# Performance work log

Measured on AMD Instinct MI355X. Metric: run time of the kernel, lower is better.

Reference implementation:

```python
import jax, jax.numpy as jnp
import numpy as np

B, S, D, H, E, K = 2, 2048, 1024, 4096, 8, 2


def setup_inputs() -> dict:
    key = jax.random.key(0)
    ks = jax.random.split(key, 5)
    x = jax.random.normal(ks[0], (B, S, D), dtype=jnp.float32)
    W = 0.02 * jax.random.normal(ks[1], (H, D), dtype=jnp.float32)
    bias = 0.02 * jax.random.normal(ks[2], (H,), dtype=jnp.float32)
    # alpha initialized near 1 (nn.Parameter(torch.ones(...)) + learned perturbation)
    alpha = 1.0 + 0.02 * jax.random.normal(ks[3], (E, D), dtype=jnp.float32)
    beta = 0.02 * jax.random.normal(ks[4], (E, D), dtype=jnp.float32)
    return {"x": x, "W": W, "bias": bias, "alpha": alpha, "beta": beta}


def reference(x, W, bias, alpha, beta):
    """MoEXLayer eval-mode forward (sparsity-aware routing + expert combine).

    x: [B,S,D], W: [H,D], bias: [H], alpha/beta: [E,D]. Returns [B,S,H].
    """
    E = alpha.shape[0]
    # --- Router: per-virtual-expert Gaussian pre-activation statistics ---
    # reconstructed_weight(alpha, beta) = W * alpha + beta  (column-wise affine)
    W_rec = W[None, :, :] * alpha[:, None, :] + beta[:, None, :]      # [E,H,D]
    mu_w = W_rec.mean(axis=1)                                          # [E,D]
    var_w = W_rec.var(axis=1)                                          # [E,D] (unbiased=False)
    mu_h = jnp.einsum('bsd,ed->bse', x, mu_w) + bias.mean()            # [B,S,E]
    sigma_h = jnp.sqrt(jnp.einsum('bsd,ed->bse', x * x, var_w) + 1e-8) # [B,S,E]
    router_logits = jax.lax.erf(mu_h / (jnp.sqrt(2.0) * sigma_h))      # [B,S,E]

    # --- Top-k routing: softmax over top-k logits, zeros elsewhere ---
    topk_vals, topk_idx = jax.lax.top_k(router_logits, K)              # [B,S,K]
    topk_w = jax.nn.softmax(topk_vals, axis=-1)                        # [B,S,K]
    router_weights = (jax.nn.one_hot(topk_idx, E, dtype=x.dtype)
                      * topk_w[..., None]).sum(axis=-2)                # [B,S,E]

    # --- Expert compute + combine (dispatch passes alpha only => beta=0) ---
    W_disp = W[None, :, :] * alpha[:, None, :]                         # [E,H,D]
    pre = jnp.einsum('bsd,ehd->bseh', x, W_disp) + bias                # [B,S,E,H]
    expert_out = jax.nn.relu(pre)
    out = jnp.einsum('bseh,bse->bsh', expert_out, router_weights)      # [B,S,H]
    return out
```

## Files before the change

kernel.cpp:

```cpp
#include <hip/hip_runtime.h>
#include <hip/hip_bf16.h>
#include <math.h>

#define DD 1024
#define HH 4096
#define EE 8
#define MTOK 4096
#define MROWS 8192

typedef __attribute__((ext_vector_type(8))) short bf16x8;
typedef __attribute__((ext_vector_type(4))) float f32x4;

__device__ __forceinline__ unsigned short f2bf(float x){
  __hip_bfloat16 h = __float2bfloat16(x);
  return *reinterpret_cast<unsigned short*>(&h);
}

__device__ __forceinline__ void gload16(const void* g, void* l){
  __builtin_amdgcn_global_load_lds((__attribute__((address_space(1))) void*)g,
                                   (__attribute__((address_space(3))) void*)l,
                                   16, 0, 0);
}

__global__ void cvtstats_kernel(const float4* __restrict__ W4, ushort4* __restrict__ Wb4,
                                float* __restrict__ pmean, float* __restrict__ pm2){
  int rc = blockIdx.x;
  int tid = threadIdx.x;
  double s0=0,s1=0,s2_=0,s3=0, q0=0,q1=0,q2=0,q3=0;
  for (int h = rc * 16; h < rc * 16 + 16; ++h){
    float4 w = W4[(size_t)h * 256 + tid];
    Wb4[(size_t)h * 256 + tid] = make_ushort4(f2bf(w.x), f2bf(w.y), f2bf(w.z), f2bf(w.w));
    s0 += w.x; q0 += (double)w.x * w.x;
    s1 += w.y; q1 += (double)w.y * w.y;
    s2_ += w.z; q2 += (double)w.z * w.z;
    s3 += w.w; q3 += (double)w.w * w.w;
  }
  int d0 = rc * DD + tid * 4;
  pmean[d0]   = (float)s0;  pm2[d0]   = (float)q0;
  pmean[d0+1] = (float)s1;  pm2[d0+1] = (float)q1;
  pmean[d0+2] = (float)s2_; pm2[d0+2] = (float)q2;
  pmean[d0+3] = (float)s3;  pm2[d0+3] = (float)q3;
}

__global__ void finalize_kernel(const float* __restrict__ pmean, const float* __restrict__ pm2,
                                const float* __restrict__ bias,
                                const float* __restrict__ alpha, const float* __restrict__ beta,
                                double* __restrict__ bmean,
                                float* __restrict__ muw, float* __restrict__ vw){
  __shared__ double redS[4][64], redQ[4][64], redB[256];
  int tid = threadIdx.x;
  int dlane = tid & 63, cq = tid >> 6;
  int d = blockIdx.x * 64 + dlane;
  double s = 0.0, s2 = 0.0;
  for (int c = cq * 64; c < cq * 64 + 64; ++c){
    s  += (double)pmean[c * DD + d];
    s2 += (double)pm2[c * DD + d];
  }
  redS[cq][dlane] = s; redQ[cq][dlane] = s2;
  __syncthreads();
  if (cq == 0){
    double S  = redS[0][dlane] + redS[1][dlane] + redS[2][dlane] + redS[3][dlane];
    double Q  = redQ[0][dlane] + redQ[1][dlane] + redQ[2][dlane] + redQ[3][dlane];
    double m = S / (double)HH;
    double v = Q / (double)HH - m * m;
    #pragma unroll
    for (int e = 0; e < EE; ++e){
      double a = (double)alpha[e * DD + d];
      muw[e * DD + d] = (float)(a * m + (double)beta[e * DD + d]);
      vw[e * DD + d]  = (float)(a * a * v);
    }
  }
  if (blockIdx.x == 0){
    double bs = 0.0;
    for (int h = tid; h < HH; h += 256) bs += (double)bias[h];
    redB[tid] = bs;
    __syncthreads();
    for (int k = 128; k > 0; k >>= 1){
      if (tid < k) redB[tid] += redB[tid + k];
      __syncthreads();
    }
    if (tid == 0) *bmean = redB[0] / (double)HH;
  }
}

__global__ __launch_bounds__(256) void router_kernel(const float4* __restrict__ x4,
                                                     const float4* __restrict__ alpha4,
                                                     const float4* __restrict__ muw4,
                                                     const float4* __restrict__ vw4,
                                                     const double* __restrict__ bmeanp,
                                                     unsigned short* __restrict__ Xs,
                                                     float2* __restrict__ wpair){
  int wv = threadIdx.x >> 6, lane = threadIdx.x & 63;
  int t = blockIdx.x * 4 + wv;
  const float4* xt = x4 + (size_t)t * 256;

  float4 xv[4];
  double mu[EE], s2[EE];
  #pragma unroll
  for (int e = 0; e < EE; ++e){ mu[e] = 0.0; s2[e] = 0.0; }

  #pragma unroll
  for (int r = 0; r < 4; ++r){
    int c = lane + 64 * r;
    float4 xf = xt[c];
    xv[r] = xf;
    float x2x = xf.x * xf.x, x2y = xf.y * xf.y, x2z = xf.z * xf.z, x2w = xf.w * xf.w;
    #pragma unroll
    for (int e = 0; e < EE; ++e){
      float4 m4 = muw4[e * 256 + c];
      float4 v4 = vw4[e * 256 + c];
      mu[e] += (double)xf.x * m4.x + (double)xf.y * m4.y
             + (double)xf.z * m4.z + (double)xf.w * m4.w;
      s2[e] += (double)x2x * v4.x + (double)x2y * v4.y
             + (double)x2z * v4.z + (double)x2w * v4.w;
    }
  }

  #pragma unroll
  for (int off = 32; off > 0; off >>= 1){
    #pragma unroll
    for (int e = 0; e < EE; ++e){
      mu[e] += __shfl_xor(mu[e], off);
      s2[e] += __shfl_xor(s2[e], off);
    }
  }

  double bm = *bmeanp;
  double z[EE];
  #pragma unroll
  for (int e = 0; e < EE; ++e){
    double m = mu[e] + bm;
    double v = s2[e] + 1e-8;
    z[e] = m / sqrt(2.0 * v);
  }
  int e1 = 0;
  #pragma unroll
  for (int e = 1; e < EE; ++e) if (z[e] > z[e1]) e1 = e;
  int e2 = -1;
  #pragma unroll
  for (int e = 0; e < EE; ++e){
    if (e == e1) continue;
    if (e2 < 0 || z[e] > z[e2]) e2 = e;
  }
  double lg1 = erf(z[e1]), lg2 = erf(z[e2]);
  double ex = exp(lg2 - lg1);
  float w1 = (float)(1.0 / (1.0 + ex));
  float w2 = (float)(ex / (1.0 + ex));
  if (lane == 0) wpair[t] = make_float2(w1, w2);

  const float4* a1 = alpha4 + (size_t)e1 * 256;
  const float4* a2 = alpha4 + (size_t)e2 * 256;
  ushort4* X1 = (ushort4*)(Xs + (size_t)(2 * t) * DD);
  ushort4* X2 = (ushort4*)(Xs + (size_t)(2 * t + 1) * DD);
  #pragma unroll
  for (int r = 0; r < 4; ++r){
    int c = lane + 64 * r;
    float4 xf = xv[r];
    float4 av = a1[c];
    X1[c] = make_ushort4(f2bf(xf.x * av.x), f2bf(xf.y * av.y),
                         f2bf(xf.z * av.z), f2bf(xf.w * av.w));
    av = a2[c];
    X2[c] = make_ushort4(f2bf(xf.x * av.x), f2bf(xf.y * av.y),
                         f2bf(xf.z * av.z), f2bf(xf.w * av.w));
  }
}

#define BM 256
#define BN 256
#define BKT 64
#define NKT (DD / BKT)
#define ASZ (BM * BKT)

__global__ __launch_bounds__(512, 1) void gemm_kernel(const unsigned short* __restrict__ Xs,
                                                      const unsigned short* __restrict__ Wb,
                                                      const float* __restrict__ bias,
                                                      const float2* __restrict__ wpair,
                                                      float* __restrict__ out){
  __shared__ __align__(16) unsigned short As[2 * ASZ];
  __shared__ __align__(16) unsigned short Bs[2 * ASZ];

  int tid = threadIdx.x, lane = tid & 63, wv = tid >> 6;
  int wr = wv >> 2, wc = wv & 3;
  int l15 = lane & 15;

  int bid = blockIdx.x;
  int ch = bid & 7, local = bid >> 3;
  int mtile = ch * 4 + (local & 3);
  int ntile = local >> 2;
  int bm0 = mtile * BM, bn0 = ntile * BN;

  int sr = tid >> 3;
  int sc = tid & 7;
  int scg = sc ^ (sr & 7);
  const unsigned short* gA = Xs + (size_t)(bm0 + sr) * DD + scg * 8;
  const unsigned short* gB = Wb + (size_t)(bn0 + sr) * DD + scg * 8;
  unsigned short* lA = As + tid * 8;
  unsigned short* lB = Bs + tid * 8;

  auto stage = [&](int kt, int slot){
    int koff = kt * BKT;
    #pragma unroll
    for (int j = 0; j < 4; ++j)
      gload16(gA + (size_t)(64 * j) * DD + koff, lA + slot * ASZ + j * 4096);
    #pragma unroll
    for (int j = 0; j < 4; ++j)
      gload16(gB + (size_t)(64 * j) * DD + koff, lB + slot * ASZ + j * 4096);
  };

  int r7 = l15 & 7;
  int posr0 = (lane >> 4) ^ r7;
  int posr1 = (4 + (lane >> 4)) ^ r7;

  f32x4 acc[8][4] = {};

  stage(0, 0);
  #pragma unroll 1
  for (int t = 0; t < NKT; ++t){
    int slot = t & 1;
    if (t < NKT - 1){
      stage(t + 1, slot ^ 1);
      asm volatile("s_waitcnt vmcnt(8)" ::: "memory");
    } else {
      asm volatile("s_waitcnt vmcnt(0)" ::: "memory");
    }
    __builtin_amdgcn_s_barrier();

    const unsigned short* Ab = As + slot * ASZ;
    const unsigned short* Bb = Bs + slot * ASZ;

    #pragma unroll
    for (int ks = 0; ks < 2; ++ks){
      int pos = ks ? posr1 : posr0;
      bf16x8 af[8], bfr[4];
      #pragma unroll
      for (int mi = 0; mi < 8; ++mi)
        af[mi] = *(const bf16x8*)(Ab + (wr * 128 + mi * 16 + l15) * BKT + pos * 8);
      #pragma unroll
      for (int ni = 0; ni < 4; ++ni)
        bfr[ni] = *(const bf16x8*)(Bb + (wc * 64 + ni * 16 + l15) * BKT + pos * 8);

      __builtin_amdgcn_s_setprio(1);
      #pragma unroll
      for (int ni = 0; ni < 4; ++ni)
        #pragma unroll
        for (int mi = 0; mi < 8; ++mi)
          acc[mi][ni] = __builtin_amdgcn_mfma_f32_16x16x32_bf16(af[mi], bfr[ni],
                                                               acc[mi][ni], 0, 0, 0);
      __builtin_amdgcn_s_setprio(0);
    }

    asm volatile("s_waitcnt lgkmcnt(0)" ::: "memory");
    __builtin_amdgcn_s_barrier();
  }

  #pragma unroll
  for (int mi = 0; mi < 8; ++mi){
    int rbase = bm0 + wr * 128 + mi * 16 + ((lane >> 4) << 2);
    #pragma unroll
    for (int jp = 0; jp < 2; ++jp){
      int gm = rbase + jp * 2;
      int tt = gm >> 1;
      float2 w = wpair[tt];
      #pragma unroll
      for (int ni = 0; ni < 4; ++ni){
        int gh = bn0 + wc * 64 + ni * 16 + l15;
        float bz = bias[gh];
        float v0 = acc[mi][ni][jp * 2]     + bz;
        float v1 = acc[mi][ni][jp * 2 + 1] + bz;
        out[(size_t)tt * HH + gh] = w.x * fmaxf(v0, 0.f) + w.y * fmaxf(v1, 0.f);
      }
    }
  }
}

extern "C" void kernel_launch(void* const* d_in, const int* in_sizes, int n_in,
                              void* d_out, int out_size, void* d_ws, size_t ws_size,
                              hipStream_t stream) {
  const float* x     = (const float*)d_in[0];
  const float* W     = (const float*)d_in[1];
  const float* bias  = (const float*)d_in[2];
  const float* alpha = (const float*)d_in[3];
  const float* beta  = (const float*)d_in[4];
  float* out = (float*)d_out;

  char* ws = (char*)d_ws;
  unsigned short* Wb = (unsigned short*)ws;
  unsigned short* Xs = (unsigned short*)(ws + (8u << 20));
  float2* wpair      = (float2*)(ws + (24u << 20));
  double* bmean      = (double*)(ws + (24u << 20) + (64u << 10));
  float* muw         = (float*)(ws + (24u << 20) + (128u << 10));
  float* vw          = muw + EE * DD;
  float* pmean       = (float*)(ws + (25u << 20));
  float* pm2         = (float*)(ws + (26u << 20));

  cvtstats_kernel<<<256, 256, 0, stream>>>((const float4*)W, (ushort4*)Wb, pmean, pm2);
  finalize_kernel<<<16, 256, 0, stream>>>(pmean, pm2, bias, alpha, beta, bmean, muw, vw);
  router_kernel<<<MTOK / 4, 256, 0, stream>>>((const float4*)x, (const float4*)alpha,
                                              (const float4*)muw, (const float4*)vw,
                                              bmean, Xs, wpair);
  gemm_kernel<<<(MROWS / BM) * (HH / BN), 512, 0, stream>>>(Xs, Wb, bias, wpair, out);
}
```

Measured before the change: 126.8 us.

## Split K tiles into half-stages and issue next loads after fragment reads

Each 64-wide K tile now sits in LDS as two 32-wide halves, laid out as [row][32] with a 4-way XOR swizzle. The next tile's global-to-LDS loads for a half are issued right after this wave reads its fragments for that half. A vmcnt(4) wait plus one barrier guards each half, and the trailing lgkmcnt wait and barrier at the end of each iteration are gone. The goal is to overlap loads with MFMA at a finer grain and cut synchronisation per tile. The risks are more LDS bank conflicts from the narrower swizzle and the cost of two barriers per tile.

```diff
diff --git a/kernel.cpp b/kernel.cpp
--- a/kernel.cpp
+++ b/kernel.cpp
@@ -169,15 +169,16 @@
 #define BN 256
 #define BKT 64
 #define NKT (DD / BKT)
-#define ASZ (BM * BKT)
+#define SLOTE 16384
+#define HALFE 8192
 
 __global__ __launch_bounds__(512, 1) void gemm_kernel(const unsigned short* __restrict__ Xs,
                                                       const unsigned short* __restrict__ Wb,
                                                       const float* __restrict__ bias,
                                                       const float2* __restrict__ wpair,
                                                       float* __restrict__ out){
-  __shared__ __align__(16) unsigned short As[2 * ASZ];
-  __shared__ __align__(16) unsigned short Bs[2 * ASZ];
+  __shared__ __align__(16) unsigned short As[2 * SLOTE];
+  __shared__ __align__(16) unsigned short Bs[2 * SLOTE];
 
   int tid = threadIdx.x, lane = tid & 63, wv = tid >> 6;
   int wr = wv >> 2, wc = wv & 3;
@@ -189,55 +190,51 @@
   int ntile = local >> 2;
   int bm0 = mtile * BM, bn0 = ntile * BN;
 
-  int sr = tid >> 3;
-  int sc = tid & 7;
-  int scg = sc ^ (sr & 7);
+  int sr = tid >> 2;
+  int sc = tid & 3;
+  int scg = sc ^ (sr & 3);
   const unsigned short* gA = Xs + (size_t)(bm0 + sr) * DD + scg * 8;
   const unsigned short* gB = Wb + (size_t)(bn0 + sr) * DD + scg * 8;
   unsigned short* lA = As + tid * 8;
   unsigned short* lB = Bs + tid * 8;
 
-  auto stage = [&](int kt, int slot){
-    int koff = kt * BKT;
-    #pragma unroll
-    for (int j = 0; j < 4; ++j)
-      gload16(gA + (size_t)(64 * j) * DD + koff, lA + slot * ASZ + j * 4096);
-    #pragma unroll
-    for (int j = 0; j < 4; ++j)
-      gload16(gB + (size_t)(64 * j) * DD + koff, lB + slot * ASZ + j * 4096);
+  auto stage = [&](int kt, int slot, int h){
+    int koff = kt * BKT + h * 32;
+    #pragma unroll
+    for (int j = 0; j < 2; ++j){
+      gload16(gA + (size_t)(128 * j) * DD + koff, lA + slot * SLOTE + h * HALFE + j * 4096);
+      gload16(gB + (size_t)(128 * j) * DD + koff, lB + slot * SLOTE + h * HALFE + j * 4096);
+    }
   };
 
-  int r7 = l15 & 7;
-  int posr0 = (lane >> 4) ^ r7;
-  int posr1 = (4 + (lane >> 4)) ^ r7;
+  int cc = ((lane >> 4) ^ (l15 & 3)) * 8;
 
   f32x4 acc[8][4] = {};
 
-  stage(0, 0);
+  stage(0, 0, 0);
+  stage(0, 0, 1);
+
   #pragma unroll 1
   for (int t = 0; t < NKT; ++t){
     int slot = t & 1;
-    if (t < NKT - 1){
-      stage(t + 1, slot ^ 1);
-      asm volatile("s_waitcnt vmcnt(8)" ::: "memory");
-    } else {
-      asm volatile("s_waitcnt vmcnt(0)" ::: "memory");
-    }
-    __builtin_amdgcn_s_barrier();
-
-    const unsigned short* Ab = As + slot * ASZ;
-    const unsigned short* Bb = Bs + slot * ASZ;
-
-    #pragma unroll
-    for (int ks = 0; ks < 2; ++ks){
-      int pos = ks ? posr1 : posr0;
+    const unsigned short* Ab = As + slot * SLOTE;
+    const unsigned short* Bb = Bs + slot * SLOTE;
+
+    #pragma unroll
+    for (int h = 0; h < 2; ++h){
+      if (t == NKT - 1 && h == 1) asm volatile("s_waitcnt vmcnt(0)" ::: "memory");
+      else                        asm volatile("s_waitcnt vmcnt(4)" ::: "memory");
+      __builtin_amdgcn_s_barrier();
+
       bf16x8 af[8], bfr[4];
       #pragma unroll
       for (int mi = 0; mi < 8; ++mi)
-        af[mi] = *(const bf16x8*)(Ab + (wr * 128 + mi * 16 + l15) * BKT + pos * 8);
+        af[mi] = *(const bf16x8*)(Ab + h * HALFE + (wr * 128 + mi * 16 + l15) * 32 + cc);
       #pragma unroll
       for (int ni = 0; ni < 4; ++ni)
-        bfr[ni] = *(const bf16x8*)(Bb + (wc * 64 + ni * 16 + l15) * BKT + pos * 8);
+        bfr[ni] = *(const bf16x8*)(Bb + h * HALFE + (wc * 64 + ni * 16 + l15) * 32 + cc);
+
+      if (t + 1 < NKT) stage(t + 1, slot ^ 1, h);
 
       __builtin_amdgcn_s_setprio(1);
       #pragma unroll
@@ -248,9 +245,6 @@
                                                                acc[mi][ni], 0, 0, 0);
       __builtin_amdgcn_s_setprio(0);
     }
-
-    asm volatile("s_waitcnt lgkmcnt(0)" ::: "memory");
-    __builtin_amdgcn_s_barrier();
   }
 
   #pragma unroll
```

New measurement: 127.4 us. No clear change (+0.5%).
